# Performance work log

Measured on AMD Instinct MI355X. Metric: run time of the kernel, lower is better.

Reference implementation:

```python
import math
import jax, jax.numpy as jnp
import numpy as np

F_MUL = 48   # multiplicity of node irreps: 48x0e + 48x1o + 48x2e
K = 16       # num_keep
P = 2        # num_poles
B = 8        # number of graphs in the batch


def _su2_cg(j1, j2, j3, m1, m2, m3):
    if m1 + m2 != m3:
        return 0.0
    f = math.factorial
    pre = ((2 * j3 + 1) * f(j3 + j1 - j2) * f(j3 - j1 + j2) * f(j1 + j2 - j3) / f(j1 + j2 + j3 + 1)) ** 0.5
    pre *= (f(j3 + m3) * f(j3 - m3) * f(j1 - m1) * f(j1 + m1) * f(j2 - m2) * f(j2 + m2)) ** 0.5
    s = 0.0
    for v in range(0, j1 + j2 - j3 + 1):
        args = [v, j1 + j2 - j3 - v, j1 - m1 - v, j2 + m2 - v, j3 - j2 + m1 + v, j3 - j1 - m2 + v]
        if min(args) < 0:
            continue
        den = 1
        for a in args:
            den *= f(a)
        s += (-1) ** v / den
    return pre * s


def _u_c2r(l):
    # complex -> real spherical-harmonics change of basis
    U = np.zeros((2 * l + 1, 2 * l + 1), dtype=complex)
    s2 = 2 ** -0.5
    for m in range(-l, l + 1):
        a = l + m
        if m > 0:
            U[a, l + m] = (-1) ** m * s2
            U[a, l - m] = s2
        elif m == 0:
            U[a, l] = 1.0
        else:
            U[a, l + m] = 1j * s2
            U[a, l - m] = -1j * (-1) ** m * s2
    return U


def _real_cg(l1, l2, l3):
    Cc = np.zeros((2 * l1 + 1, 2 * l2 + 1, 2 * l3 + 1), dtype=complex)
    for a, m1 in enumerate(range(-l1, l1 + 1)):
        for b, m2 in enumerate(range(-l2, l2 + 1)):
            for c, m3 in enumerate(range(-l3, l3 + 1)):
                Cc[a, b, c] = _su2_cg(l1, l2, l3, m1, m2, m3)
    U1, U2, U3 = _u_c2r(l1), _u_c2r(l2), _u_c2r(l3)
    C = np.einsum('ap,bq,cr,pqr->abc', np.conj(U1), np.conj(U2), U3, Cc)
    C = C.imag if np.abs(C.imag).max() > np.abs(C.real).max() else C.real
    nrm = np.linalg.norm(C)
    return np.asarray(C / max(nrm, 1e-12), dtype=np.float32)  # unit Frobenius norm (e3nn w3j convention)

# uvu tensor-product paths (l1, l2, l3): node x node -> {0e,1o,2e}
PATHS = [(0, 0, 0), (0, 1, 1), (0, 2, 2), (1, 0, 1), (1, 1, 0), (1, 1, 2), (1, 2, 1), (2, 0, 2), (2, 1, 1), (2, 2, 0), (2, 2, 2)]
CG = {lls: jnp.asarray(_real_cg(*lls)) for lls in set(PATHS) | {(1, 1, 2)}}


def setup_inputs() -> dict:
    key = jax.random.key(0)
    ks = jax.random.split(key, 12)
    n, Fm = 512, F_MUL
    return {
        'node_feats': jax.random.normal(ks[0], (n, 9 * Fm), jnp.float32),
        'W_lin0': jax.random.normal(ks[1], (Fm, Fm), jnp.float32),
        'W_lin1': jax.random.normal(ks[2], (Fm, Fm), jnp.float32),
        'W_lin2': jax.random.normal(ks[3], (Fm, Fm), jnp.float32),
        'tp_w': jax.random.normal(ks[4], (len(PATHS), Fm, Fm), jnp.float32),
        'W_out0': jax.random.normal(ks[5], (3 * Fm, K * Fm), jnp.float32),
        'W_out1': jax.random.normal(ks[6], (4 * Fm, K * Fm), jnp.float32),
        'W_out2': jax.random.normal(ks[7], (4 * Fm, K * Fm), jnp.float32),
        'Wt0': jax.random.normal(ks[8], (K, 2), jnp.float32),
        'Wt1': jax.random.normal(ks[9], (K, 1), jnp.float32),
        'Wt2': jax.random.normal(ks[10], (K, 1), jnp.float32),
        'batch': jnp.sort(jax.random.randint(ks[11], (n,), 0, B)),
        'max_nodes': 128,
    }


def reference(node_feats, W_lin0, W_lin1, W_lin2, tp_w, W_out0, W_out1, W_out2, Wt0, Wt1, Wt2, batch, max_nodes):
    n = node_feats.shape[0]
    Fm = F_MUL
    # split into l=0,1,2 blocks: [n, F, 2l+1]
    x = [node_feats[:, :Fm].reshape(n, Fm, 1),
         node_feats[:, Fm:4 * Fm].reshape(n, Fm, 3),
         node_feats[:, 4 * Fm:9 * Fm].reshape(n, Fm, 5)]
    sF = np.float32(Fm) ** -0.5
    # linear_diag: per-l channel mixing
    y = [jnp.einsum('nui,uv->nvi', xl, W) * sF for xl, W in zip(x, (W_lin0, W_lin1, W_lin2))]
    # conv_tp_diag: uvu tensor product of y with itself, one slot per path
    outs = {0: [], 1: [], 2: []}
    for p, (l1, l2, l3) in enumerate(PATHS):
        a = jnp.einsum('nvk,uv->nuk', y[l2], tp_w[p]) * sF
        outs[l3].append(jnp.einsum('num,nuk,mkc->nuc', y[l1], a, CG[(l1, l2, l3)]))
    h = []
    for l, Wo in ((0, W_out0), (1, W_out1), (2, W_out2)):
        o = jnp.concatenate(outs[l], axis=1)  # [n, n_paths*F, 2l+1]
        h.append(jnp.einsum('nui,uv->nvi', o, Wo) * np.float32(o.shape[1]) ** -0.5)  # [n, K*F, 2l+1]
    # reshape_irreps: [n, K*F, 2l+1] -> [n, F, K, 2l+1]
    r = [hl.reshape(n, K, Fm, 2 * l + 1).transpose(0, 2, 1, 3) for l, hl in enumerate(h)]
    sK = np.float32(K) ** -0.5
    g0 = jnp.einsum('nfki,ko->nfoi', r[0], Wt0) * sK  # [n,F,2,1]
    g1 = jnp.einsum('nfki,ko->nfoi', r[1], Wt1) * sK  # [n,F,1,3]
    g2 = jnp.einsum('nfki,ko->nfoi', r[2], Wt2) * sK  # [n,F,1,5]
    a0, a1 = g0[:, :, 0, 0], g0[:, :, 1, 0]
    v, d = g1[:, :, 0, :], g2[:, :, 0, :]
    # symmetric 4x4 block per (node, feature): [[a0, v], [v, a1*I/sqrt3 + CG(1,1,2).d]]
    S = a1[..., None, None] * (jnp.eye(3, dtype=a1.dtype) * np.float32(3) ** -0.5) \
        + jnp.einsum('nfm,ijm->nfij', d, CG[(1, 1, 2)])
    top = jnp.concatenate([a0[..., None, None], v[:, :, None, :]], axis=-1)  # [n,F,1,4]
    bot = jnp.concatenate([v[..., None], S], axis=-1)                        # [n,F,3,4]
    M = jnp.concatenate([top, bot], axis=2)                                  # [n,F,4,4]
    D = 4 * Fm
    big = jnp.einsum('nfij,fg->nfigj', M, jnp.eye(Fm, dtype=M.dtype)).reshape(n, D, D)
    H = jnp.broadcast_to(big[:, None], (n, P, D, D))  # repeat over poles
    # to_dense_batch
    counts = jax.ops.segment_sum(jnp.ones((n,), jnp.int32), batch, num_segments=B)
    starts = jnp.concatenate([jnp.zeros((1,), jnp.int32), jnp.cumsum(counts)[:-1]])
    pos = jnp.arange(n) - starts[batch]
    return jnp.zeros((B, max_nodes, P, D, D), H.dtype).at[batch, pos].set(H, mode='drop')
```

## Files before the change

kernel.cpp:

```cpp
#include <hip/hip_runtime.h>


#define FM 48

__device__ const int ZOFF[11] = {0,48,192,432,480,624,768,1008,1056,1200,1440};
__device__ const int NOFF[11] = {0,48,192,432,576,624,864,1008,1248,1392,1440};
__device__ const int OOFF[11] = {0,144,720,288,48,960,432,1200,576,96,1440};
__device__ const int PL2[11]  = {0,1,2,0,1,1,2,0,1,2,2};
__device__ const int PL3[11]  = {0,1,2,1,0,2,1,2,1,0,2};

#define R10f 0.31622776601683794f
#define R30f 0.18257418583505536f
#define A70f 0.23904572186687872f
#define B70f 0.11952286093343936f
#define T70f 0.20701966780270626f

__device__ const float CG112[3][3][5] = {
  {{0,0,-R30f,0,-R10f},{0,R10f,0,0,0},{R10f,0,0,0,0}},
  {{0,R10f,0,0,0},{0,0,2.0f*R30f,0,0},{0,0,0,R10f,0}},
  {{R10f,0,0,0,0},{0,0,0,R10f,0},{0,0,-R30f,0,R10f}}
};

__device__ const float CG121[3][5][3] = {
  {{0,0,-R10f},{0,-R10f,0},{R30f,0,0},{0,0,0},{R10f,0,0}},
  {{0,0,0},{-R10f,0,0},{0,-2.0f*R30f,0},{0,0,-R10f},{0,0,0}},
  {{-R10f,0,0},{0,0,0},{0,0,R30f},{0,-R10f,0},{0,0,-R10f}}
};

__device__ const float CG222[5][5][5] = {
  {{0,0,A70f,0,0},{0,0,0,-T70f,0},{A70f,0,0,0,0},{0,-T70f,0,0,0},{0,0,0,0,0}},
  {{0,0,0,-T70f,0},{0,0,-B70f,0,T70f},{0,-B70f,0,0,0},{-T70f,0,0,0,0},{0,T70f,0,0,0}},
  {{A70f,0,0,0,0},{0,-B70f,0,0,0},{0,0,-A70f,0,0},{0,0,0,-B70f,0},{0,0,0,0,A70f}},
  {{0,-T70f,0,0,0},{-T70f,0,0,0,0},{0,0,0,-B70f,0},{0,0,-B70f,0,-T70f},{0,0,0,-T70f,0}},
  {{0,0,0,0,0},{0,T70f,0,0,0},{0,0,0,0,A70f},{0,0,0,-T70f,0},{0,0,A70f,0,0}}
};

__global__ void weff_kernel(const float* __restrict__ Wo0, const float* __restrict__ Wo1,
                            const float* __restrict__ Wo2, const float* __restrict__ Wt0,
                            const float* __restrict__ Wt1, const float* __restrict__ Wt2,
                            float* __restrict__ weff0, float* __restrict__ weff1,
                            float* __restrict__ weff2) {
  int idx = blockIdx.x * 256 + threadIdx.x;
  const float s0  = 1.0f / 48.0f;
  const float s12 = 0.018042195912175807f;
  if (idx < 144*48*2) {
    int o = idx & 1, f = (idx >> 1) % 48, u = idx / 96;
    float acc = 0.0f;
    for (int k = 0; k < 16; ++k) acc += Wo0[u*768 + k*48 + f] * Wt0[k*2 + o];
    weff0[idx] = acc * s0;
  } else if (idx < 144*48*2 + 192*48) {
    int j = idx - 144*48*2; int f = j % 48, u = j / 48;
    float acc = 0.0f;
    for (int k = 0; k < 16; ++k) acc += Wo1[u*768 + k*48 + f] * Wt1[k];
    weff1[j] = acc * s12;
  } else if (idx < 144*48*2 + 2*192*48) {
    int j = idx - 144*48*2 - 192*48; int f = j % 48, u = j / 48;
    float acc = 0.0f;
    for (int k = 0; k < 16; ++k) acc += Wo2[u*768 + k*48 + f] * Wt2[k];
    weff2[j] = acc * s12;
  }
}

__global__ void starts_kernel(const int* __restrict__ batch, int n, int* __restrict__ starts) {
  int b = threadIdx.x;
  if (b < 8) {
    int c = 0;
    for (int i = 0; i < n; ++i) c += (batch[i] < b) ? 1 : 0;
    starts[b] = c;
  }
}

__global__ __launch_bounds__(256) void node_kernel(
    const float* __restrict__ feats, const float* __restrict__ Wl0,
    const float* __restrict__ Wl1, const float* __restrict__ Wl2,
    const float* __restrict__ tpw, const float* __restrict__ weff0,
    const float* __restrict__ weff1, const float* __restrict__ weff2,
    const int* __restrict__ batch, const int* __restrict__ starts,
    float* __restrict__ out, int max_nodes) {
  const int node = blockIdx.x;
  const int tid = threadIdx.x;
  const float sF = 0.14433756729740643f;

  __shared__ float xs[432];
  __shared__ float ys[432];
  __shared__ float zs[1680];
  __shared__ float os[1680];
  __shared__ float gs[480];

  const float* fr = feats + node * 432;
  for (int t = tid; t < 432; t += 256) xs[t] = fr[t];
  __syncthreads();

  for (int t = tid; t < 432; t += 256) {
    float acc = 0.0f;
    if (t < 48) {
      int v = t;
      for (int u = 0; u < 48; ++u) acc += xs[u] * Wl0[u*48 + v];
    } else if (t < 192) {
      int j = t - 48, v = j / 3, i = j % 3;
      for (int u = 0; u < 48; ++u) acc += xs[48 + u*3 + i] * Wl1[u*48 + v];
    } else {
      int j = t - 192, v = j / 5, i = j % 5;
      for (int u = 0; u < 48; ++u) acc += xs[192 + u*5 + i] * Wl2[u*48 + v];
    }
    ys[t] = acc * sF;
  }
  __syncthreads();

  for (int t = tid; t < 1680; t += 256) {
    int p = 10; while (ZOFF[p] > t) --p;
    int j = t - ZOFF[p];
    int l2 = PL2[p], K2 = 2*l2 + 1;
    int u = j / K2, k = j % K2;
    const float* tw = tpw + p*2304 + u*48;
    const float* yy = ys + (l2 == 0 ? 0 : (l2 == 1 ? 48 : 192));
    float acc = 0.0f;
    for (int v = 0; v < 48; ++v) acc += tw[v] * yy[v*K2 + k];
    zs[t] = acc * sF;
  }
  __syncthreads();

  for (int t = tid; t < 1680; t += 256) {
    int p = 10; while (NOFF[p] > t) --p;
    int j = t - NOFF[p];
    int K3 = 2*PL3[p] + 1;
    int u = j / K3, c = j % K3;
    const float* zp = zs + ZOFF[p];
    float acc = 0.0f;
    switch (p) {
      case 0: acc = ys[u] * zp[u]; break;
      case 1: acc = 0.5773502691896258f * ys[u] * zp[u*3 + c]; break;
      case 2: acc = 0.4472135954999579f * ys[u] * zp[u*5 + c]; break;
      case 3: acc = 0.5773502691896258f * ys[48 + u*3 + c] * zp[u]; break;
      case 4: { float s = 0.0f;
                for (int m = 0; m < 3; ++m) s += ys[48 + u*3 + m] * zp[u*3 + m];
                acc = -0.5773502691896258f * s; } break;
      case 5: for (int m = 0; m < 3; ++m)
                for (int k = 0; k < 3; ++k)
                  acc += ys[48 + u*3 + m] * zp[u*3 + k] * CG112[m][k][c];
              break;
      case 6: for (int m = 0; m < 3; ++m)
                for (int k = 0; k < 5; ++k)
                  acc += ys[48 + u*3 + m] * zp[u*5 + k] * CG121[m][k][c];
              break;
      case 7: acc = 0.4472135954999579f * ys[192 + u*5 + c] * zp[u]; break;
      case 8: for (int m = 0; m < 5; ++m)
                for (int k = 0; k < 3; ++k)
                  acc += ys[192 + u*5 + m] * zp[u*3 + k] * CG121[k][m][c];
              break;
      case 9: { float s = 0.0f;
                for (int m = 0; m < 5; ++m) s += ys[192 + u*5 + m] * zp[u*5 + m];
                acc = 0.4472135954999579f * s; } break;
      default: for (int m = 0; m < 5; ++m)
                 for (int k = 0; k < 5; ++k)
                   acc += ys[192 + u*5 + m] * zp[u*5 + k] * CG222[m][k][c];
               break;
    }
    os[OOFF[p] + u*K3 + c] = acc;
  }
  __syncthreads();

  for (int t = tid; t < 480; t += 256) {
    float acc = 0.0f;
    if (t < 96) {
      int f = t >> 1, o = t & 1;
      for (int u = 0; u < 144; ++u) acc += os[u] * weff0[u*96 + f*2 + o];
    } else if (t < 240) {
      int j = t - 96, f = j / 3, i = j % 3;
      for (int u = 0; u < 192; ++u) acc += os[144 + u*3 + i] * weff1[u*48 + f];
    } else {
      int j = t - 240, f = j / 5, m = j % 5;
      for (int u = 0; u < 192; ++u) acc += os[720 + u*5 + m] * weff2[u*48 + f];
    }
    gs[t] = acc;
  }
  __syncthreads();

  int b = batch[node];
  int pos = node - starts[b];
  if (pos >= max_nodes) return;
  size_t base = (size_t)b * (size_t)max_nodes * 73728u + (size_t)pos * 73728u;
  const float R3i = 0.5773502691896258f;
  for (int t = tid; t < 384; t += 256) {
    int p = t / 192, j = t % 192, f = j >> 2, i = j & 3;
    float a0 = gs[f*2 + 0], a1 = gs[f*2 + 1];
    float v0 = gs[96 + f*3 + 0], v1 = gs[96 + f*3 + 1], v2 = gs[96 + f*3 + 2];
    float d0 = gs[240 + f*5 + 0], d1 = gs[240 + f*5 + 1], d2 = gs[240 + f*5 + 2];
    float d3 = gs[240 + f*5 + 3], d4 = gs[240 + f*5 + 4];
    float m0, m1, m2, m3;
    if (i == 0)      { m0 = a0; m1 = v0; m2 = v1; m3 = v2; }
    else if (i == 1) { m0 = v0; m1 = a1*R3i - R30f*d2 - R10f*d4; m2 = R10f*d1; m3 = R10f*d0; }
    else if (i == 2) { m0 = v1; m1 = R10f*d1; m2 = a1*R3i + 2.0f*R30f*d2; m3 = R10f*d3; }
    else             { m0 = v2; m1 = R10f*d0; m2 = R10f*d3; m3 = a1*R3i - R30f*d2 + R10f*d4; }
    float4 val = make_float4(m0, m1, m2, m3);
    *(float4*)(out + base + (size_t)p*36864u + (size_t)(f*4 + i)*192u + (size_t)(f*4)) = val;
  }
}

extern "C" void kernel_launch(void* const* d_in, const int* in_sizes, int n_in,
                              void* d_out, int out_size, void* d_ws, size_t ws_size,
                              hipStream_t stream) {
  const float* feats = (const float*)d_in[0];
  const float* Wl0   = (const float*)d_in[1];
  const float* Wl1   = (const float*)d_in[2];
  const float* Wl2   = (const float*)d_in[3];
  const float* tpw   = (const float*)d_in[4];
  const float* Wo0   = (const float*)d_in[5];
  const float* Wo1   = (const float*)d_in[6];
  const float* Wo2   = (const float*)d_in[7];
  const float* Wt0   = (const float*)d_in[8];
  const float* Wt1   = (const float*)d_in[9];
  const float* Wt2   = (const float*)d_in[10];
  const int*   batch = (const int*)d_in[11];

  int n = in_sizes[0] / 432;
  int max_nodes = out_size / (8 * 2 * 192 * 192);

  float* ws    = (float*)d_ws;
  float* weff0 = ws;
  float* weff1 = ws + 13824;
  float* weff2 = ws + 23040;
  int*   starts = (int*)(ws + 32256);

  hipMemsetAsync(d_out, 0, (size_t)out_size * sizeof(float), stream);
  weff_kernel<<<126, 256, 0, stream>>>(Wo0, Wo1, Wo2, Wt0, Wt1, Wt2, weff0, weff1, weff2);
  starts_kernel<<<1, 64, 0, stream>>>(batch, n, starts);
  node_kernel<<<n, 256, 0, stream>>>(feats, Wl0, Wl1, Wl2, tpw, weff0, weff1, weff2,
                                     batch, starts, (float*)d_out, max_nodes);
}
```

Measured before the change: 411.1 us.

## Replace memset and scatter with fused zero-fill kernel; transpose weff for contiguous reads

```diff
diff --git a/kernel.cpp b/kernel.cpp
--- a/kernel.cpp
+++ b/kernel.cpp
@@ -1,7 +1,5 @@
 #include <hip/hip_runtime.h>
 
-
-#define FM 48
 
 __device__ const int ZOFF[11] = {0,48,192,432,480,624,768,1008,1056,1200,1440};
 __device__ const int NOFF[11] = {0,48,192,432,576,624,864,1008,1248,1392,1440};
@@ -43,18 +41,19 @@
   int idx = blockIdx.x * 256 + threadIdx.x;
   const float s0  = 1.0f / 48.0f;
   const float s12 = 0.018042195912175807f;
-  if (idx < 144*48*2) {
-    int o = idx & 1, f = (idx >> 1) % 48, u = idx / 96;
+  if (idx < 13824) {
+    int u = idx % 144, fo = idx / 144;
+    int f = fo >> 1, o = fo & 1;
     float acc = 0.0f;
     for (int k = 0; k < 16; ++k) acc += Wo0[u*768 + k*48 + f] * Wt0[k*2 + o];
     weff0[idx] = acc * s0;
-  } else if (idx < 144*48*2 + 192*48) {
-    int j = idx - 144*48*2; int f = j % 48, u = j / 48;
+  } else if (idx < 23040) {
+    int j = idx - 13824; int u = j % 192, f = j / 192;
     float acc = 0.0f;
     for (int k = 0; k < 16; ++k) acc += Wo1[u*768 + k*48 + f] * Wt1[k];
     weff1[j] = acc * s12;
-  } else if (idx < 144*48*2 + 2*192*48) {
-    int j = idx - 144*48*2 - 192*48; int f = j % 48, u = j / 48;
+  } else if (idx < 32256) {
+    int j = idx - 23040; int u = j % 192, f = j / 192;
     float acc = 0.0f;
     for (int k = 0; k < 16; ++k) acc += Wo2[u*768 + k*48 + f] * Wt2[k];
     weff2[j] = acc * s12;
@@ -63,7 +62,7 @@
 
 __global__ void starts_kernel(const int* __restrict__ batch, int n, int* __restrict__ starts) {
   int b = threadIdx.x;
-  if (b < 8) {
+  if (b < 9) {
     int c = 0;
     for (int i = 0; i < n; ++i) c += (batch[i] < b) ? 1 : 0;
     starts[b] = c;
@@ -75,8 +74,7 @@
     const float* __restrict__ Wl1, const float* __restrict__ Wl2,
     const float* __restrict__ tpw, const float* __restrict__ weff0,
     const float* __restrict__ weff1, const float* __restrict__ weff2,
-    const int* __restrict__ batch, const int* __restrict__ starts,
-    float* __restrict__ out, int max_nodes) {
+    float* __restrict__ mblk) {
   const int node = blockIdx.x;
   const int tid = threadIdx.x;
   const float sF = 0.14433756729740643f;
@@ -163,37 +161,58 @@
   for (int t = tid; t < 480; t += 256) {
     float acc = 0.0f;
     if (t < 96) {
-      int f = t >> 1, o = t & 1;
-      for (int u = 0; u < 144; ++u) acc += os[u] * weff0[u*96 + f*2 + o];
+      const float* w = weff0 + t * 144;
+      for (int u = 0; u < 144; ++u) acc += os[u] * w[u];
     } else if (t < 240) {
       int j = t - 96, f = j / 3, i = j % 3;
-      for (int u = 0; u < 192; ++u) acc += os[144 + u*3 + i] * weff1[u*48 + f];
+      const float* w = weff1 + f * 192;
+      for (int u = 0; u < 192; ++u) acc += os[144 + u*3 + i] * w[u];
     } else {
       int j = t - 240, f = j / 5, m = j % 5;
-      for (int u = 0; u < 192; ++u) acc += os[720 + u*5 + m] * weff2[u*48 + f];
+      const float* w = weff2 + f * 192;
+      for (int u = 0; u < 192; ++u) acc += os[720 + u*5 + m] * w[u];
     }
     gs[t] = acc;
   }
   __syncthreads();
 
-  int b = batch[node];
-  int pos = node - starts[b];
-  if (pos >= max_nodes) return;
-  size_t base = (size_t)b * (size_t)max_nodes * 73728u + (size_t)pos * 73728u;
-  const float R3i = 0.5773502691896258f;
-  for (int t = tid; t < 384; t += 256) {
-    int p = t / 192, j = t % 192, f = j >> 2, i = j & 3;
+  if (tid < 192) {
+    int f = tid >> 2, i = tid & 3;
     float a0 = gs[f*2 + 0], a1 = gs[f*2 + 1];
     float v0 = gs[96 + f*3 + 0], v1 = gs[96 + f*3 + 1], v2 = gs[96 + f*3 + 2];
     float d0 = gs[240 + f*5 + 0], d1 = gs[240 + f*5 + 1], d2 = gs[240 + f*5 + 2];
     float d3 = gs[240 + f*5 + 3], d4 = gs[240 + f*5 + 4];
+    const float R3i = 0.5773502691896258f;
     float m0, m1, m2, m3;
     if (i == 0)      { m0 = a0; m1 = v0; m2 = v1; m3 = v2; }
     else if (i == 1) { m0 = v0; m1 = a1*R3i - R30f*d2 - R10f*d4; m2 = R10f*d1; m3 = R10f*d0; }
     else if (i == 2) { m0 = v1; m1 = R10f*d1; m2 = a1*R3i + 2.0f*R30f*d2; m3 = R10f*d3; }
     else             { m0 = v2; m1 = R10f*d0; m2 = R10f*d3; m3 = a1*R3i - R30f*d2 + R10f*d4; }
-    float4 val = make_float4(m0, m1, m2, m3);
-    *(float4*)(out + base + (size_t)p*36864u + (size_t)(f*4 + i)*192u + (size_t)(f*4)) = val;
+    *(float4*)(mblk + node * 768 + (tid << 2)) = make_float4(m0, m1, m2, m3);
+  }
+}
+
+__global__ __launch_bounds__(256) void fill_kernel(const float* __restrict__ mblk,
+                                                   const int* __restrict__ starts,
+                                                   float* __restrict__ out) {
+  const int tid = threadIdx.x;
+  const int b = blockIdx.z, pos = blockIdx.y;
+  const int s0 = starts[b], s1 = starts[b + 1];
+  const int node = s0 + pos;
+  const bool valid = node < s1;
+  float* dst = out + (size_t)(b * gridDim.y + pos) * 73728u;
+  const float4 zero = make_float4(0.f, 0.f, 0.f, 0.f);
+  const int base = blockIdx.x * 2048 + tid;
+  #pragma unroll
+  for (int k = 0; k < 8; ++k) {
+    int idx = base + k * 256;
+    int j = idx % 48;
+    int row = (idx / 48) % 192;
+    float4 val = zero;
+    if (valid && j == (row >> 2)) {
+      val = *(const float4*)(mblk + node * 768 + (row << 2));
+    }
+    *(float4*)(dst + (size_t)idx * 4) = val;
   }
 }
 
@@ -216,15 +235,15 @@
   int n = in_sizes[0] / 432;
   int max_nodes = out_size / (8 * 2 * 192 * 192);
 
-  float* ws    = (float*)d_ws;
-  float* weff0 = ws;
-  float* weff1 = ws + 13824;
-  float* weff2 = ws + 23040;
+  float* ws     = (float*)d_ws;
+  float* weff0  = ws;
+  float* weff1  = ws + 13824;
+  float* weff2  = ws + 23040;
   int*   starts = (int*)(ws + 32256);
-
-  hipMemsetAsync(d_out, 0, (size_t)out_size * sizeof(float), stream);
+  float* mblk   = ws + 32272;
+
   weff_kernel<<<126, 256, 0, stream>>>(Wo0, Wo1, Wo2, Wt0, Wt1, Wt2, weff0, weff1, weff2);
   starts_kernel<<<1, 64, 0, stream>>>(batch, n, starts);
-  node_kernel<<<n, 256, 0, stream>>>(feats, Wl0, Wl1, Wl2, tpw, weff0, weff1, weff2,
-                                     batch, starts, (float*)d_out, max_nodes);
-}
+  node_kernel<<<n, 256, 0, stream>>>(feats, Wl0, Wl1, Wl2, tpw, weff0, weff1, weff2, mblk);
+  fill_kernel<<<dim3(9, max_nodes, 8), 256, 0, stream>>>(mblk, starts, (float*)d_out);
+}
```

Result: no change. 412.7 us (+0.4%).
